# Kernel optimization log

Hardware: AMD Instinct MI355X
Metric: run time of the kernel (lower is better)

Reference implementation:

```python
import jax, jax.numpy as jnp
import numpy as np

B, T, N = 16, 2048, 24
K, C_IN, C0, C1 = 3, 1, 64, 64
KS, PRED_LEN = 3, 24
EPS = 1e-5


def _norm_laplacian(adj):
    # L = D^-1/2 A^T D^-1/2 (matches scipy path: (A D^-1/2)^T D^-1/2)
    d = adj.sum(axis=1)
    dis = jnp.where(d > 0, 1.0 / jnp.sqrt(d), 0.0)
    return dis[:, None] * adj.T * dis[None, :]


def _cheb_stack(L, k_terms):
    polys = [jnp.eye(N, dtype=L.dtype), L]
    for _ in range(2, k_terms):
        polys.append(2.0 * L @ polys[-1] - polys[-2])
    return jnp.stack(polys[:k_terms])  # (K, N, N)


def _causal_conv(x, w, b, dilation):
    ks = w.shape[-1]
    pad = (ks - 1) * dilation
    x = jnp.pad(x, ((0, 0), (0, 0), (0, 0), (pad, 0)))
    y = jax.lax.conv_general_dilated(
        x, w, window_strides=(1, 1), padding='VALID',
        rhs_dilation=(1, dilation),
        dimension_numbers=('NCHW', 'OIHW', 'NCHW'))
    return y + b[None, :, None, None]


def _bn(x, g, be):
    # training-mode batch norm over (B, N, T) per channel
    mu = x.mean(axis=(0, 2, 3), keepdims=True)
    var = x.var(axis=(0, 2, 3), keepdims=True)
    return g[None, :, None, None] * (x - mu) * jax.lax.rsqrt(var + EPS) + be[None, :, None, None]


def setup_inputs() -> dict:
    key = jax.random.key(0)
    ks = jax.random.split(key, 16)
    s = 0.05
    return {
        'batch_x': jax.random.normal(ks[0], (B, T, N), jnp.float32),
        'adj': jax.random.uniform(ks[1], (N, N), jnp.float32),
        'theta': jax.random.normal(ks[2], (K, C_IN, C0), jnp.float32),  # Theta per Cheb term
        'w1a': jax.random.normal(ks[3], (C0, C0, 1, KS), jnp.float32) * s,
        'b1a': jnp.zeros((C0,), jnp.float32),
        'g1a': jnp.ones((C0,), jnp.float32), 'be1a': jnp.zeros((C0,), jnp.float32),
        'w1b': jax.random.normal(ks[4], (C0, C0, 1, KS), jnp.float32) * s,
        'b1b': jnp.zeros((C0,), jnp.float32),
        'g1b': jnp.ones((C0,), jnp.float32), 'be1b': jnp.zeros((C0,), jnp.float32),
        'w2a': jax.random.normal(ks[5], (C1, C0, 1, KS), jnp.float32) * s,
        'b2a': jnp.zeros((C1,), jnp.float32),
        'g2a': jnp.ones((C1,), jnp.float32), 'be2a': jnp.zeros((C1,), jnp.float32),
        'w2b': jax.random.normal(ks[6], (C1, C1, 1, KS), jnp.float32) * s,
        'b2b': jnp.zeros((C1,), jnp.float32),
        'g2b': jnp.ones((C1,), jnp.float32), 'be2b': jnp.zeros((C1,), jnp.float32),
        'w_end': jax.random.normal(ks[7], (C1 // 2, C1, 1, 1), jnp.float32) * s,
        'b_end': jnp.zeros((C1 // 2,), jnp.float32),
        'w_end1': jax.random.normal(ks[8], (1, C1 // 2, 1, 2), jnp.float32) * s,
        'b_end1': jnp.zeros((1,), jnp.float32),
    }


def reference(batch_x, adj, theta,
              w1a, b1a, g1a, be1a, w1b, b1b, g1b, be1b,
              w2a, b2a, g2a, be2a, w2b, b2b, g2b, be2b,
              w_end, b_end, w_end1, b_end1):
    # (B, T, N) -> (B, 1, N, T)
    x = jnp.transpose(batch_x, (0, 2, 1))[:, None, :, :]

    # --- Cheb_conv: fused over K terms and all timesteps ---
    L = _norm_laplacian(adj)
    Tk = _cheb_stack(L, K)                       # (K, N, N)
    xp = jnp.transpose(x, (0, 2, 1, 3))          # (B, N, C_in, T)
    # out[b,o,n,t] = sum_{k,m,c} xp[b,m,c,t] Tk[k,m,n] theta[k,c,o]
    gc = jnp.einsum('bmct,kmn,kco->bont', xp, Tk, theta)  # (B, C0, N, T)

    # --- TCN block 1 (dilation 1), residual is identity (C0 == C0) ---
    h = jax.nn.relu(_bn(_causal_conv(gc, w1a, b1a, 1), g1a, be1a))
    h = jax.nn.relu(_bn(_causal_conv(h, w1b, b1b, 1), g1b, be1b))
    out0 = jax.nn.relu(h + gc)

    # --- TCN block 2 (dilation 2), residual identity (C0 == C1), no final relu ---
    h = jax.nn.relu(_bn(_causal_conv(out0, w2a, b2a, 2), g2a, be2a))
    h = jax.nn.relu(_bn(_causal_conv(h, w2b, b2b, 2), g2b, be2b))
    out = h + out0                               # (B, C1, N, T)

    # --- head: 1x1 conv + relu, then (1,2) valid conv -> 1 channel ---
    e = jax.lax.conv_general_dilated(out, w_end, (1, 1), 'VALID',
                                     dimension_numbers=('NCHW', 'OIHW', 'NCHW'))
    e = jax.nn.relu(e + b_end[None, :, None, None])
    e = jax.lax.conv_general_dilated(e, w_end1, (1, 1), 'VALID',
                                     dimension_numbers=('NCHW', 'OIHW', 'NCHW'))
    e = e + b_end1[None, :, None, None]          # (B, 1, N, T-1)
    e = e[:, 0, :, -PRED_LEN:]                   # (B, N, pred_len)
    return jnp.transpose(e, (0, 2, 1))           # (B, pred_len, N)
```

## Files before the change

kernel.cpp:

```cpp
#include <hip/hip_runtime.h>
#include <cmath>

#define TPB 256

typedef __attribute__((ext_vector_type(8)))  short short8;
typedef __attribute__((ext_vector_type(16))) float float16;

static constexpr int  BB   = 16;
static constexpr int  TDIM = 2048;
static constexpr int  NN   = 24;
static constexpr int  P    = BB * NN;
static constexpr int  C    = 64;
static constexpr int  TILE = 256;
static constexpr int  NBT  = TDIM / TILE;
static constexpr int  NSHARD = 64;
static constexpr float INV_CNT = 1.0f / 786432.0f;
static constexpr int  XPITCH = 72;

static constexpr size_t OFF_TK    = 0;
static constexpr size_t OFF_WEFF  = 6912;
static constexpr size_t OFF_WFRAG = 9216;
static constexpr size_t OFF_ST    = 82944;
static constexpr size_t OFF_BNAB  = 214016;
static constexpr size_t OFF_O0    = 216320;
static constexpr size_t OFF_YT    = 2673920;
static constexpr size_t OFF_S     = 5131520;
static constexpr size_t OFF_YA    = 14568704;
static constexpr size_t OFF_YB    = 115232000;

__device__ __forceinline__ unsigned short f2bf(float f) {
    unsigned int i = __float_as_uint(f);
    i += 0x7FFFu + ((i >> 16) & 1u);
    return (unsigned short)(i >> 16);
}
__device__ __forceinline__ float bf2f(unsigned short u) {
    return __uint_as_float((unsigned)u << 16);
}

__global__ __launch_bounds__(TPB)
void prep_kernel(const float* __restrict__ adj, const float* __restrict__ theta,
                 const float* __restrict__ w1a,
                 const float* __restrict__ w1b, const float* __restrict__ w2a,
                 const float* __restrict__ w2b,
                 float* __restrict__ tk, float* __restrict__ weff,
                 unsigned short* __restrict__ wf, float* __restrict__ stats)
{
    const int tid = threadIdx.x;
    if (blockIdx.x < 144) {
        int e = blockIdx.x * TPB + tid;
        int conv = e / 12288, r = e % 12288;
        int oh = r / 6144; r %= 6144;
        int kc = r / 512;  r %= 512;
        int lane = r / 8;
        int jj = r % 8;
        int o = oh * 32 + (lane & 31);
        int K = kc * 16 + (lane >> 5) * 8 + jj;
        int j = K / 64, c2 = K % 64;
        const float* w = (conv == 0) ? w1b : ((conv == 1) ? w2a : w2b);
        wf[e] = f2bf(w[(o * 64 + c2) * 3 + j]);
        return;
    }

    __shared__ float disl[24];
    __shared__ float Ll[576];
    __shared__ float T2l[576];

    for (int e = tid; e < 4 * 2 * 64 * NSHARD; e += TPB) stats[e] = 0.f;

    if (tid < 24) {
        float d = 0.f;
        for (int j = 0; j < 24; ++j) d += adj[tid * 24 + j];
        disl[tid] = (d > 0.f) ? 1.0f / sqrtf(d) : 0.f;
    }
    __syncthreads();
    for (int e = tid; e < 576; e += TPB) {
        int i = e / 24, j = e % 24;
        Ll[e] = disl[i] * adj[j * 24 + i] * disl[j];
    }
    __syncthreads();
    for (int e = tid; e < 576; e += TPB) {
        int i = e / 24, j = e % 24;
        float a = 0.f;
        for (int m = 0; m < 24; ++m) a += Ll[i * 24 + m] * Ll[m * 24 + j];
        T2l[e] = 2.f * a - ((i == j) ? 1.f : 0.f);
    }
    __syncthreads();
    for (int e = tid; e < 576; e += TPB) {
        int i = e / 24, j = e % 24;
        tk[e]        = (i == j) ? 1.f : 0.f;
        tk[576 + e]  = Ll[e];
        tk[1152 + e] = T2l[e];
    }
    for (int e = tid; e < 576; e += TPB) {
        int o = e / 9, k = (e % 9) / 3, j = e % 3;
        float a = 0.f;
        for (int c2 = 0; c2 < 64; ++c2)
            a += w1a[(o * 64 + c2) * 3 + j] * theta[k * 64 + c2];
        weff[(k * 3 + j) * 64 + o] = a;
    }
}

__global__ __launch_bounds__(TPB)
void bnprep_kernel(const float* __restrict__ stats, const float* __restrict__ g,
                   const float* __restrict__ be, float2* __restrict__ ab)
{
    const int tid = threadIdx.x;
    const int ch = tid >> 2, q = tid & 3;
    float s1 = 0.f, s2 = 0.f;
    #pragma unroll
    for (int u = 0; u < 16; ++u) {
        int sh = q * 16 + u;
        s1 += stats[ch * 64 + sh];
        s2 += stats[(64 + ch) * 64 + sh];
    }
    s1 += __shfl_xor(s1, 1); s1 += __shfl_xor(s1, 2);
    s2 += __shfl_xor(s2, 1); s2 += __shfl_xor(s2, 2);
    if (q == 0) {
        float mu  = s1 * INV_CNT;
        float var = s2 * INV_CNT - mu * mu;
        float a = g[ch] * (1.0f / sqrtf(var + 1e-5f));
        ab[ch] = make_float2(a, be[ch] - mu * a);
    }
}

__global__ __launch_bounds__(TPB)
void s_kernel(const float* __restrict__ bx, const float* __restrict__ tk,
              float* __restrict__ sbuf)
{
    __shared__ float bxs[256 * 25];
    __shared__ float tkl[1728];
    const int tid = threadIdx.x;
    const int b  = blockIdx.x >> 3;
    const int t0 = (blockIdx.x & 7) * 256;

    for (int e = tid; e < 1728; e += TPB) tkl[e] = tk[e];
    for (int e = tid; e < 256 * 24; e += TPB) {
        int t = e / 24, m = e % 24;
        bxs[t * 25 + m] = bx[((long)b * TDIM + t0 + t) * NN + m];
    }
    __syncthreads();

    const int t = tid;
    for (int k = 0; k < 3; ++k) {
        float acc[24];
        #pragma unroll
        for (int n = 0; n < 24; ++n) acc[n] = 0.f;
        for (int m = 0; m < 24; ++m) {
            float xb = bxs[t * 25 + m];
            const float* tr = tkl + k * 576 + m * 24;
            #pragma unroll
            for (int n = 0; n < 24; ++n) acc[n] = fmaf(xb, tr[n], acc[n]);
        }
        for (int n = 0; n < 24; ++n)
            sbuf[((long)k * P + b * NN + n) * TDIM + t0 + t] = acc[n];
    }
}

__global__ __launch_bounds__(TPB)
void stats1a_kernel(const float* __restrict__ sbuf, const float* __restrict__ weff,
                    float* __restrict__ statsOut)
{
    __shared__ float4 ssl4[3 * 66];
    __shared__ float4 wl4[144];
    __shared__ float  part[4][2][64];
    const int tid = threadIdx.x;
    const int blk = blockIdx.x;
    const int p  = blk >> 3;
    const int t0 = (blk & 7) * TILE;

    for (int e = tid; e < 576; e += TPB) ((float*)wl4)[e] = weff[e];
    for (int e = tid; e < 3 * 65; e += TPB) {
        int k = e / 65, u4 = e % 65;
        int t = t0 - 4 + u4 * 4;
        float4 v = make_float4(0.f, 0.f, 0.f, 0.f);
        if (t >= 0) v = *(const float4*)(sbuf + ((long)k * P + p) * TDIM + t);
        ssl4[k * 66 + u4] = v;
    }
    __syncthreads();

    const int oq = tid & 7;
    const int tq = tid >> 3;
    float acc[8][8];
    #pragma unroll
    for (int i = 0; i < 8; ++i)
        #pragma unroll
        for (int ti = 0; ti < 8; ++ti) acc[i][ti] = 0.f;

    #pragma unroll
    for (int k = 0; k < 3; ++k) {
        float4 x0 = ssl4[k * 66 + tq * 2];
        float4 x1 = ssl4[k * 66 + tq * 2 + 1];
        float4 x2 = ssl4[k * 66 + tq * 2 + 2];
        float xv[12] = { x0.x,x0.y,x0.z,x0.w, x1.x,x1.y,x1.z,x1.w, x2.x,x2.y,x2.z,x2.w };
        #pragma unroll
        for (int j = 0; j < 3; ++j) {
            float4 w0 = wl4[(k * 3 + j) * 16 + oq * 2];
            float4 w1 = wl4[(k * 3 + j) * 16 + oq * 2 + 1];
            float wv[8] = { w0.x,w0.y,w0.z,w0.w, w1.x,w1.y,w1.z,w1.w };
            #pragma unroll
            for (int i = 0; i < 8; ++i)
                #pragma unroll
                for (int ti = 0; ti < 8; ++ti)
                    acc[i][ti] = fmaf(wv[i], xv[ti + 2 + j], acc[i][ti]);
        }
    }

    float s1v[8], s2v[8];
    #pragma unroll
    for (int i = 0; i < 8; ++i) {
        float a1 = 0.f, a2 = 0.f;
        #pragma unroll
        for (int ti = 0; ti < 8; ++ti) { a1 += acc[i][ti]; a2 += acc[i][ti] * acc[i][ti]; }
        s1v[i] = a1; s2v[i] = a2;
    }
    #pragma unroll
    for (int m = 8; m < 64; m <<= 1) {
        #pragma unroll
        for (int i = 0; i < 8; ++i) {
            s1v[i] += __shfl_xor(s1v[i], m);
            s2v[i] += __shfl_xor(s2v[i], m);
        }
    }
    const int wave = tid >> 6, lane = tid & 63;
    if (lane < 8) {
        #pragma unroll
        for (int i = 0; i < 8; ++i) {
            part[wave][0][oq * 8 + i] = s1v[i];
            part[wave][1][oq * 8 + i] = s2v[i];
        }
    }
    __syncthreads();
    if (tid < 128) {
        int s = tid >> 6, o = tid & 63;
        float tot = part[0][s][o] + part[1][s][o] + part[2][s][o] + part[3][s][o];
        atomicAdd(&statsOut[(s * 64 + o) * NSHARD + (blk & 63)], tot);
    }
}

template<int MODE>
__global__ __launch_bounds__(TPB)
void conv_mfma(const float* __restrict__ sbuf, const unsigned short* __restrict__ yin,
               unsigned short* __restrict__ yout, float* __restrict__ ytail,
               const unsigned short* __restrict__ wf, const float* __restrict__ weff,
               const float2* __restrict__ bnab, float* __restrict__ statsOut,
               const float* __restrict__ theta, float* __restrict__ o0s)
{
    __shared__ unsigned short Xl[260 * XPITCH];
    __shared__ float4 ssl4[3 * 66];
    __shared__ float  weffl[576];
    __shared__ float  thl[192];
    __shared__ float2 abl[64];
    __shared__ float  parts[4][8][8][2];

    const int tid  = threadIdx.x;
    const int lane = tid & 63;
    const int w    = tid >> 6;
    const int oh   = w & 1;
    const int l31  = lane & 31;
    const int h    = lane >> 5;
    const int blk  = blockIdx.x;
    const int p    = blk >> 3;
    const int tile = blk & 7;
    const int t0   = tile * TILE;
    const float* sslf = (const float*)ssl4;

    short8 af[12];
    #pragma unroll
    for (int kc = 0; kc < 12; ++kc)
        af[kc] = *((const short8*)wf + (oh * 12 + kc) * 64 + lane);

    if (tid < 64) abl[tid] = bnab[tid];
    if (MODE == 0)
        for (int e = tid; e < 576; e += TPB) weffl[e] = weff[e];
    if (MODE == 1)
        for (int e = tid; e < 192; e += TPB) thl[e] = theta[e];
    if (MODE <= 1) {
        for (int e = tid; e < 3 * 66; e += TPB) {
            int k = e / 66, u4 = e % 66;
            int t = t0 - 8 + u4 * 4;
            float4 v = make_float4(0.f, 0.f, 0.f, 0.f);
            if (t >= 0) v = *(const float4*)(sbuf + ((long)k * P + p) * TDIM + t);
            ssl4[k * 66 + u4] = v;
        }
    }
    __syncthreads();

    for (int e = tid; e < 260 * 8; e += TPB) {
        const int tt = e >> 3, cb = e & 7;
        const int t = t0 - 4 + tt;
        float xv[8];
        if (t < 0) {
            #pragma unroll
            for (int r = 0; r < 8; ++r) xv[r] = 0.f;
        } else if (MODE == 0) {
            float sv[9];
            #pragma unroll
            for (int k = 0; k < 3; ++k)
                #pragma unroll
                for (int j = 0; j < 3; ++j)
                    sv[k * 3 + j] = sslf[k * 264 + tt + 2 + j];
            #pragma unroll
            for (int r = 0; r < 8; ++r) {
                int c = cb * 8 + r;
                float raw = 0.f;
                #pragma unroll
                for (int q = 0; q < 9; ++q)
                    raw = fmaf(weffl[q * 64 + c], sv[q], raw);
                float2 ab = abl[c];
                xv[r] = fmaxf(fmaf(ab.x, raw, ab.y), 0.f);
            }
        } else {
            short8 yv8 = *(const short8*)(yin + ((long)p * TDIM + t) * 64 + cb * 8);
            float gcb[3];
            if (MODE == 1) {
                gcb[0] = sslf[      tt + 4];
                gcb[1] = sslf[264 + tt + 4];
                gcb[2] = sslf[528 + tt + 4];
            }
            #pragma unroll
            for (int r = 0; r < 8; ++r) {
                int c = cb * 8 + r;
                float2 ab = abl[c];
                float v = bf2f((unsigned short)yv8[r]);
                float hh = fmaxf(fmaf(ab.x, v, ab.y), 0.f);
                if (MODE == 1) {
                    float gc = thl[c] * gcb[0] + thl[64 + c] * gcb[1] + thl[128 + c] * gcb[2];
                    hh = fmaxf(hh + gc, 0.f);
                }
                xv[r] = hh;
            }
        }
        if (MODE == 1 && tile == 7 && tt >= 235) {
            #pragma unroll
            for (int r = 0; r < 8; ++r)
                o0s[(long)p * 1600 + (cb * 8 + r) * 25 + (tt - 235)] = xv[r];
        }
        short8 pk;
        #pragma unroll
        for (int r = 0; r < 8; ++r) pk[r] = (short)f2bf(xv[r]);
        *(short8*)(Xl + tt * XPITCH + cb * 8) = pk;
    }
    __syncthreads();

    float16 acc[4];
    #pragma unroll
    for (int i = 0; i < 4; ++i)
        #pragma unroll
        for (int r = 0; r < 16; ++r) acc[i][r] = 0.f;

    const int tqb = (w >> 1) * 4;
    #pragma unroll
    for (int kc = 0; kc < 12; ++kc) {
        const int j = kc >> 2;
        const int roff = (MODE == 0) ? (2 + j) : (2 * j);
        const int cbase = (kc & 3) * 16 + h * 8;
        #pragma unroll
        for (int i = 0; i < 4; ++i) {
            int row = (tqb + i) * 32 + l31 + roff;
            short8 bfr = *(const short8*)(Xl + row * XPITCH + cbase);
            acc[i] = __builtin_amdgcn_mfma_f32_32x32x16_bf16(af[kc], bfr, acc[i], 0, 0, 0);
        }
    }

    __syncthreads();

    if (MODE == 2 && tile == 7) {
        #pragma unroll
        for (int i = 0; i < 4; ++i) {
            int tg = t0 + (tqb + i) * 32 + l31;
            if (tg >= TDIM - 25) {
                #pragma unroll
                for (int r = 0; r < 16; ++r) {
                    int o = oh * 32 + (r & 3) + 8 * (r >> 2) + 4 * h;
                    ytail[((long)p * C + o) * 25 + (tg - (TDIM - 25))] = acc[i][r];
                }
            }
        }
    }

    #pragma unroll
    for (int i = 0; i < 4; ++i) {
        int tl = (tqb + i) * 32 + l31;
        #pragma unroll
        for (int q = 0; q < 4; ++q) {
            int ob = oh * 32 + 8 * q + 4 * h;
            ushort4 pk;
            pk.x = f2bf(acc[i][4 * q + 0]);
            pk.y = f2bf(acc[i][4 * q + 1]);
            pk.z = f2bf(acc[i][4 * q + 2]);
            pk.w = f2bf(acc[i][4 * q + 3]);
            *(ushort4*)(Xl + tl * XPITCH + ob) = pk;
        }
    }
    __syncthreads();

    const int cb = tid & 7;
    float s1[8], s2[8];
    #pragma unroll
    for (int r = 0; r < 8; ++r) { s1[r] = 0.f; s2[r] = 0.f; }
    for (int e = tid; e < 2048; e += TPB) {
        int tt = e >> 3;
        short8 v = *(const short8*)(Xl + tt * XPITCH + cb * 8);
        if (MODE <= 1)
            *(short8*)(yout + ((long)p * TDIM + t0 + tt) * 64 + cb * 8) = v;
        #pragma unroll
        for (int r = 0; r < 8; ++r) {
            float f = bf2f((unsigned short)v[r]);
            s1[r] += f;
            s2[r] = fmaf(f, f, s2[r]);
        }
    }
    #pragma unroll
    for (int m = 8; m <= 32; m <<= 1) {
        #pragma unroll
        for (int r = 0; r < 8; ++r) {
            s1[r] += __shfl_xor(s1[r], m);
            s2[r] += __shfl_xor(s2[r], m);
        }
    }
    if (lane < 8) {
        #pragma unroll
        for (int r = 0; r < 8; ++r) {
            parts[w][lane][r][0] = s1[r];
            parts[w][lane][r][1] = s2[r];
        }
    }
    __syncthreads();
    if (tid < 64) {
        int o = tid, cbo = o >> 3, r = o & 7;
        float t1 = parts[0][cbo][r][0] + parts[1][cbo][r][0]
                 + parts[2][cbo][r][0] + parts[3][cbo][r][0];
        float t2 = parts[0][cbo][r][1] + parts[1][cbo][r][1]
                 + parts[2][cbo][r][1] + parts[3][cbo][r][1];
        atomicAdd(&statsOut[o * NSHARD + (blk & 63)], t1);
        atomicAdd(&statsOut[(64 + o) * NSHARD + (blk & 63)], t2);
    }
}

__global__ __launch_bounds__(TPB)
void end_kernel(const float* __restrict__ ytail, const float* __restrict__ o0s,
                const float2* __restrict__ bnab, const float* __restrict__ w_end,
                const float* __restrict__ b_end, const float* __restrict__ w_end1,
                const float* __restrict__ b_end1, float* __restrict__ out)
{
    __shared__ float2 abl[64];
    __shared__ float outl[64 * 25];
    __shared__ float e1l[32 * 25];
    __shared__ float wendl[2048];
    const int tid = threadIdx.x;
    const int p = blockIdx.x;
    const int b = p / 24, n = p % 24;

    if (tid < 64) abl[tid] = bnab[tid];
    for (int e = tid; e < 2048; e += TPB) wendl[e] = w_end[e];
    __syncthreads();

    for (int e = tid; e < 1600; e += TPB) {
        int c = e / 25, tau = e % 25;
        float v = ytail[((long)p * C + c) * 25 + tau];
        float2 ab = abl[c];
        outl[e] = fmaxf(ab.x * v + ab.y, 0.f) + o0s[(long)p * 1600 + e];
    }
    __syncthreads();
    for (int e = tid; e < 800; e += TPB) {
        int q = e / 25, tau = e % 25;
        float a = b_end[q];
        for (int c = 0; c < 64; ++c)
            a = fmaf(wendl[q * 64 + c], outl[c * 25 + tau], a);
        e1l[e] = fmaxf(a, 0.f);
    }
    __syncthreads();
    if (tid < 24) {
        float a = b_end1[0];
        #pragma unroll
        for (int q = 0; q < 32; ++q)
            a += w_end1[q * 2] * e1l[q * 25 + tid] + w_end1[q * 2 + 1] * e1l[q * 25 + tid + 1];
        out[((long)b * 24 + tid) * 24 + n] = a;
    }
}

extern "C" void kernel_launch(void* const* d_in, const int* in_sizes, int n_in,
                              void* d_out, int out_size, void* d_ws, size_t ws_size,
                              hipStream_t stream)
{
    (void)in_sizes; (void)n_in; (void)out_size; (void)ws_size;
    const float* bx    = (const float*)d_in[0];
    const float* adj   = (const float*)d_in[1];
    const float* theta = (const float*)d_in[2];
    const float* w1a   = (const float*)d_in[3];
    const float* g1a   = (const float*)d_in[5];
    const float* be1a  = (const float*)d_in[6];
    const float* w1b   = (const float*)d_in[7];
    const float* g1b   = (const float*)d_in[9];
    const float* be1b  = (const float*)d_in[10];
    const float* w2a   = (const float*)d_in[11];
    const float* g2a   = (const float*)d_in[13];
    const float* be2a  = (const float*)d_in[14];
    const float* w2b   = (const float*)d_in[15];
    const float* g2b   = (const float*)d_in[17];
    const float* be2b  = (const float*)d_in[18];
    const float* wend  = (const float*)d_in[19];
    const float* bend  = (const float*)d_in[20];
    const float* wend1 = (const float*)d_in[21];
    const float* bend1 = (const float*)d_in[22];

    char* ws = (char*)d_ws;
    float*          tk    = (float*)(ws + OFF_TK);
    float*          weff  = (float*)(ws + OFF_WEFF);
    unsigned short* wf    = (unsigned short*)(ws + OFF_WFRAG);
    float*          stats = (float*)(ws + OFF_ST);
    float2*         bnab  = (float2*)(ws + OFF_BNAB);
    float*          o0s   = (float*)(ws + OFF_O0);
    float*          ytail = (float*)(ws + OFF_YT);
    float*          sb    = (float*)(ws + OFF_S);
    unsigned short* yA    = (unsigned short*)(ws + OFF_YA);
    unsigned short* yB    = (unsigned short*)(ws + OFF_YB);

    prep_kernel   <<<145, TPB, 0, stream>>>(adj, theta, w1a, w1b, w2a, w2b,
                                            tk, weff, wf, stats);
    s_kernel      <<<128, TPB, 0, stream>>>(bx, tk, sb);
    stats1a_kernel<<<P * NBT, TPB, 0, stream>>>(sb, weff, stats);
    bnprep_kernel <<<1, TPB, 0, stream>>>(stats,         g1a, be1a, bnab);

    conv_mfma<0><<<P * NBT, TPB, 0, stream>>>(
        sb, nullptr, yA, nullptr, wf, weff,
        bnab, stats + 8192, nullptr, nullptr);
    bnprep_kernel <<<1, TPB, 0, stream>>>(stats + 8192,  g1b, be1b, bnab + 64);

    conv_mfma<1><<<P * NBT, TPB, 0, stream>>>(
        sb, yA, yB, nullptr, wf + 12288, nullptr,
        bnab + 64, stats + 16384, theta, o0s);
    bnprep_kernel <<<1, TPB, 0, stream>>>(stats + 16384, g2a, be2a, bnab + 128);

    conv_mfma<2><<<P * NBT, TPB, 0, stream>>>(
        sb, yB, nullptr, ytail, wf + 24576, nullptr,
        bnab + 128, stats + 24576, nullptr, nullptr);
    bnprep_kernel <<<1, TPB, 0, stream>>>(stats + 24576, g2b, be2b, bnab + 192);

    end_kernel<<<P, TPB, 0, stream>>>(ytail, o0s, bnab + 192,
                                      wend, bend, wend1, bend1, (float*)d_out);
}
```

Measured before the change: 359.5 us.

## Fold BN stat finalisation into consumers, split s_kernel, streamline conv epilogues

Removes the four single-block bnprep launches; each conv_mfma and end_kernel block now reduces the sharded BN statistics itself into shared memory. s_kernel is split across the three Chebyshev terms for more blocks. bf16 packing uses a perm-based round-to-nearest that drops the ties-to-even correction. The final conv mode computes BN statistics directly from MFMA accumulators in registers instead of staging through LDS. This trades redundant per-block stat reductions for fewer launches and serialization points.

```diff
diff --git a/kernel.cpp b/kernel.cpp
--- a/kernel.cpp
+++ b/kernel.cpp
@@ -21,7 +21,6 @@
 static constexpr size_t OFF_WEFF  = 6912;
 static constexpr size_t OFF_WFRAG = 9216;
 static constexpr size_t OFF_ST    = 82944;
-static constexpr size_t OFF_BNAB  = 214016;
 static constexpr size_t OFF_O0    = 216320;
 static constexpr size_t OFF_YT    = 2673920;
 static constexpr size_t OFF_S     = 5131520;
@@ -35,6 +34,34 @@
 }
 __device__ __forceinline__ float bf2f(unsigned short u) {
     return __uint_as_float((unsigned)u << 16);
+}
+__device__ __forceinline__ unsigned pk2bf(float a, float b) {
+    unsigned ua = __float_as_uint(a) + 0x8000u;
+    unsigned ub = __float_as_uint(b) + 0x8000u;
+    return __builtin_amdgcn_perm(ub, ua, 0x07060302u);
+}
+
+__device__ __forceinline__
+void bn_from_stats(const float* __restrict__ statsIn, const float* __restrict__ g,
+                   const float* __restrict__ be, float2* abl, int tid)
+{
+    const int ch = tid >> 2, q = tid & 3;
+    float s1 = 0.f, s2 = 0.f;
+    #pragma unroll
+    for (int u = 0; u < 4; ++u) {
+        float4 a = *(const float4*)(statsIn + tid * 16 + u * 4);
+        float4 b = *(const float4*)(statsIn + 4096 + tid * 16 + u * 4);
+        s1 += a.x + a.y + a.z + a.w;
+        s2 += b.x + b.y + b.z + b.w;
+    }
+    s1 += __shfl_xor(s1, 1); s1 += __shfl_xor(s1, 2);
+    s2 += __shfl_xor(s2, 1); s2 += __shfl_xor(s2, 2);
+    if (q == 0) {
+        float mu  = s1 * INV_CNT;
+        float var = s2 * INV_CNT - mu * mu;
+        float a = g[ch] * (1.0f / sqrtf(var + 1e-5f));
+        abl[ch] = make_float2(a, be[ch] - mu * a);
+    }
 }
 
 __global__ __launch_bounds__(TPB)
@@ -65,7 +92,7 @@
     __shared__ float Ll[576];
     __shared__ float T2l[576];
 
-    for (int e = tid; e < 4 * 2 * 64 * NSHARD; e += TPB) stats[e] = 0.f;
+    for (int e = tid; e < 4 * 8192; e += TPB) stats[e] = 0.f;
 
     if (tid < 24) {
         float d = 0.f;
@@ -101,39 +128,19 @@
 }
 
 __global__ __launch_bounds__(TPB)
-void bnprep_kernel(const float* __restrict__ stats, const float* __restrict__ g,
-                   const float* __restrict__ be, float2* __restrict__ ab)
-{
-    const int tid = threadIdx.x;
-    const int ch = tid >> 2, q = tid & 3;
-    float s1 = 0.f, s2 = 0.f;
-    #pragma unroll
-    for (int u = 0; u < 16; ++u) {
-        int sh = q * 16 + u;
-        s1 += stats[ch * 64 + sh];
-        s2 += stats[(64 + ch) * 64 + sh];
-    }
-    s1 += __shfl_xor(s1, 1); s1 += __shfl_xor(s1, 2);
-    s2 += __shfl_xor(s2, 1); s2 += __shfl_xor(s2, 2);
-    if (q == 0) {
-        float mu  = s1 * INV_CNT;
-        float var = s2 * INV_CNT - mu * mu;
-        float a = g[ch] * (1.0f / sqrtf(var + 1e-5f));
-        ab[ch] = make_float2(a, be[ch] - mu * a);
-    }
-}
-
-__global__ __launch_bounds__(TPB)
 void s_kernel(const float* __restrict__ bx, const float* __restrict__ tk,
               float* __restrict__ sbuf)
 {
     __shared__ float bxs[256 * 25];
-    __shared__ float tkl[1728];
+    __shared__ float tkl[576];
     const int tid = threadIdx.x;
-    const int b  = blockIdx.x >> 3;
-    const int t0 = (blockIdx.x & 7) * 256;
-
-    for (int e = tid; e < 1728; e += TPB) tkl[e] = tk[e];
+    const int blk = blockIdx.x;
+    const int b  = blk / 24;
+    const int r  = blk % 24;
+    const int k  = r >> 3;
+    const int t0 = (r & 7) * 256;
+
+    for (int e = tid; e < 576; e += TPB) tkl[e] = tk[k * 576 + e];
     for (int e = tid; e < 256 * 24; e += TPB) {
         int t = e / 24, m = e % 24;
         bxs[t * 25 + m] = bx[((long)b * TDIM + t0 + t) * NN + m];
@@ -141,19 +148,17 @@
     __syncthreads();
 
     const int t = tid;
-    for (int k = 0; k < 3; ++k) {
-        float acc[24];
-        #pragma unroll
-        for (int n = 0; n < 24; ++n) acc[n] = 0.f;
-        for (int m = 0; m < 24; ++m) {
-            float xb = bxs[t * 25 + m];
-            const float* tr = tkl + k * 576 + m * 24;
-            #pragma unroll
-            for (int n = 0; n < 24; ++n) acc[n] = fmaf(xb, tr[n], acc[n]);
-        }
-        for (int n = 0; n < 24; ++n)
-            sbuf[((long)k * P + b * NN + n) * TDIM + t0 + t] = acc[n];
-    }
+    float acc[24];
+    #pragma unroll
+    for (int n = 0; n < 24; ++n) acc[n] = 0.f;
+    for (int m = 0; m < 24; ++m) {
+        float xb = bxs[t * 25 + m];
+        const float* tr = tkl + m * 24;
+        #pragma unroll
+        for (int n = 0; n < 24; ++n) acc[n] = fmaf(xb, tr[n], acc[n]);
+    }
+    for (int n = 0; n < 24; ++n)
+        sbuf[((long)k * P + b * NN + n) * TDIM + t0 + t] = acc[n];
 }
 
 __global__ __launch_bounds__(TPB)
@@ -166,7 +171,7 @@
     const int tid = threadIdx.x;
     const int blk = blockIdx.x;
     const int p  = blk >> 3;
-    const int t0 = (blk & 7) * TILE;
+    const int t0 = (blk & 7) * 256;
 
     for (int e = tid; e < 576; e += TPB) ((float*)wl4)[e] = weff[e];
     for (int e = tid; e < 3 * 65; e += TPB) {
@@ -242,15 +247,16 @@
 void conv_mfma(const float* __restrict__ sbuf, const unsigned short* __restrict__ yin,
                unsigned short* __restrict__ yout, float* __restrict__ ytail,
                const unsigned short* __restrict__ wf, const float* __restrict__ weff,
-               const float2* __restrict__ bnab, float* __restrict__ statsOut,
+               const float* __restrict__ statsIn, const float* __restrict__ g,
+               const float* __restrict__ be, float* __restrict__ statsOut,
                const float* __restrict__ theta, float* __restrict__ o0s)
 {
     __shared__ unsigned short Xl[260 * XPITCH];
-    __shared__ float4 ssl4[3 * 66];
-    __shared__ float  weffl[576];
-    __shared__ float  thl[192];
+    __shared__ float  ssl[(MODE <= 1) ? 3 * 264 : 4];
+    __shared__ float  weffl[(MODE == 0) ? 576 : 4];
+    __shared__ float  thl[(MODE == 1) ? 192 : 4];
     __shared__ float2 abl[64];
-    __shared__ float  parts[4][8][8][2];
+    __shared__ float  parts[(MODE <= 1) ? 4 * 8 * 8 * 2 : 4 * 2 * 16 * 2];
 
     const int tid  = threadIdx.x;
     const int lane = tid & 63;
@@ -262,14 +268,14 @@
     const int p    = blk >> 3;
     const int tile = blk & 7;
     const int t0   = tile * TILE;
-    const float* sslf = (const float*)ssl4;
 
     short8 af[12];
     #pragma unroll
     for (int kc = 0; kc < 12; ++kc)
         af[kc] = *((const short8*)wf + (oh * 12 + kc) * 64 + lane);
 
-    if (tid < 64) abl[tid] = bnab[tid];
+    bn_from_stats(statsIn, g, be, abl, tid);
+
     if (MODE == 0)
         for (int e = tid; e < 576; e += TPB) weffl[e] = weff[e];
     if (MODE == 1)
@@ -280,11 +286,13 @@
             int t = t0 - 8 + u4 * 4;
             float4 v = make_float4(0.f, 0.f, 0.f, 0.f);
             if (t >= 0) v = *(const float4*)(sbuf + ((long)k * P + p) * TDIM + t);
-            ssl4[k * 66 + u4] = v;
-        }
-    }
-    __syncthreads();
-
+            *(float4*)(ssl + k * 264 + u4 * 4) = v;
+        }
+    }
+    __syncthreads();
+
+    const unsigned short* yinb = (MODE >= 1)
+        ? (yin + ((long)p * TDIM + t0 - 4) * 64) : nullptr;
     for (int e = tid; e < 260 * 8; e += TPB) {
         const int tt = e >> 3, cb = e & 7;
         const int t = t0 - 4 + tt;
@@ -298,7 +306,7 @@
             for (int k = 0; k < 3; ++k)
                 #pragma unroll
                 for (int j = 0; j < 3; ++j)
-                    sv[k * 3 + j] = sslf[k * 264 + tt + 2 + j];
+                    sv[k * 3 + j] = ssl[k * 264 + tt + 2 + j];
             #pragma unroll
             for (int r = 0; r < 8; ++r) {
                 int c = cb * 8 + r;
@@ -310,12 +318,12 @@
                 xv[r] = fmaxf(fmaf(ab.x, raw, ab.y), 0.f);
             }
         } else {
-            short8 yv8 = *(const short8*)(yin + ((long)p * TDIM + t) * 64 + cb * 8);
+            short8 yv8 = *(const short8*)(yinb + (long)e * 8);
             float gcb[3];
             if (MODE == 1) {
-                gcb[0] = sslf[      tt + 4];
-                gcb[1] = sslf[264 + tt + 4];
-                gcb[2] = sslf[528 + tt + 4];
+                gcb[0] = ssl[      tt + 4];
+                gcb[1] = ssl[264 + tt + 4];
+                gcb[2] = ssl[528 + tt + 4];
             }
             #pragma unroll
             for (int r = 0; r < 8; ++r) {
@@ -335,10 +343,12 @@
             for (int r = 0; r < 8; ++r)
                 o0s[(long)p * 1600 + (cb * 8 + r) * 25 + (tt - 235)] = xv[r];
         }
-        short8 pk;
-        #pragma unroll
-        for (int r = 0; r < 8; ++r) pk[r] = (short)f2bf(xv[r]);
-        *(short8*)(Xl + tt * XPITCH + cb * 8) = pk;
+        uint4 pk;
+        pk.x = pk2bf(xv[0], xv[1]);
+        pk.y = pk2bf(xv[2], xv[3]);
+        pk.z = pk2bf(xv[4], xv[5]);
+        pk.w = pk2bf(xv[6], xv[7]);
+        *(uint4*)(Xl + tt * XPITCH + cb * 8) = pk;
     }
     __syncthreads();
 
@@ -362,84 +372,124 @@
         }
     }
 
-    __syncthreads();
-
-    if (MODE == 2 && tile == 7) {
+    if (MODE <= 1) {
+        __syncthreads();
+
         #pragma unroll
         for (int i = 0; i < 4; ++i) {
-            int tg = t0 + (tqb + i) * 32 + l31;
-            if (tg >= TDIM - 25) {
-                #pragma unroll
-                for (int r = 0; r < 16; ++r) {
-                    int o = oh * 32 + (r & 3) + 8 * (r >> 2) + 4 * h;
-                    ytail[((long)p * C + o) * 25 + (tg - (TDIM - 25))] = acc[i][r];
+            int tl = (tqb + i) * 32 + l31;
+            #pragma unroll
+            for (int q = 0; q < 4; ++q) {
+                int ob = oh * 32 + 8 * q + 4 * h;
+                uint2 pk;
+                pk.x = pk2bf(acc[i][4 * q + 0], acc[i][4 * q + 1]);
+                pk.y = pk2bf(acc[i][4 * q + 2], acc[i][4 * q + 3]);
+                *(uint2*)(Xl + tl * XPITCH + ob) = pk;
+            }
+        }
+        __syncthreads();
+
+        const int cb = tid & 7;
+        unsigned short* youtb = yout + ((long)p * TDIM + t0) * 64;
+        float s1[8], s2[8];
+        #pragma unroll
+        for (int r = 0; r < 8; ++r) { s1[r] = 0.f; s2[r] = 0.f; }
+        for (int e = tid; e < 2048; e += TPB) {
+            int tt = e >> 3;
+            uint4 v = *(const uint4*)(Xl + tt * XPITCH + cb * 8);
+            *(uint4*)(youtb + (long)e * 8) = v;
+            unsigned uu[4] = { v.x, v.y, v.z, v.w };
+            #pragma unroll
+            for (int q = 0; q < 4; ++q) {
+                float f0 = __uint_as_float(uu[q] << 16);
+                float f1 = __uint_as_float(uu[q] & 0xFFFF0000u);
+                s1[2 * q]     += f0;  s2[2 * q]     = fmaf(f0, f0, s2[2 * q]);
+                s1[2 * q + 1] += f1;  s2[2 * q + 1] = fmaf(f1, f1, s2[2 * q + 1]);
+            }
+        }
+        #pragma unroll
+        for (int m = 8; m <= 32; m <<= 1) {
+            #pragma unroll
+            for (int r = 0; r < 8; ++r) {
+                s1[r] += __shfl_xor(s1[r], m);
+                s2[r] += __shfl_xor(s2[r], m);
+            }
+        }
+        if (lane < 8) {
+            #pragma unroll
+            for (int r = 0; r < 8; ++r) {
+                parts[((w * 8 + lane) * 8 + r) * 2 + 0] = s1[r];
+                parts[((w * 8 + lane) * 8 + r) * 2 + 1] = s2[r];
+            }
+        }
+        __syncthreads();
+        if (tid < 64) {
+            int o = tid, cbo = o >> 3, r = o & 7;
+            float t1 = 0.f, t2 = 0.f;
+            #pragma unroll
+            for (int ww = 0; ww < 4; ++ww) {
+                t1 += parts[((ww * 8 + cbo) * 8 + r) * 2 + 0];
+                t2 += parts[((ww * 8 + cbo) * 8 + r) * 2 + 1];
+            }
+            atomicAdd(&statsOut[o * NSHARD + (blk & 63)], t1);
+            atomicAdd(&statsOut[(64 + o) * NSHARD + (blk & 63)], t2);
+        }
+    } else {
+        if (tile == 7) {
+            #pragma unroll
+            for (int i = 0; i < 4; ++i) {
+                int tg = t0 + (tqb + i) * 32 + l31;
+                if (tg >= TDIM - 25) {
+                    #pragma unroll
+                    for (int r = 0; r < 16; ++r) {
+                        int o = oh * 32 + (r & 3) + 8 * (r >> 2) + 4 * h;
+                        ytail[((long)p * C + o) * 25 + (tg - (TDIM - 25))] = acc[i][r];
+                    }
                 }
             }
         }
-    }
-
-    #pragma unroll
-    for (int i = 0; i < 4; ++i) {
-        int tl = (tqb + i) * 32 + l31;
-        #pragma unroll
-        for (int q = 0; q < 4; ++q) {
-            int ob = oh * 32 + 8 * q + 4 * h;
-            ushort4 pk;
-            pk.x = f2bf(acc[i][4 * q + 0]);
-            pk.y = f2bf(acc[i][4 * q + 1]);
-            pk.z = f2bf(acc[i][4 * q + 2]);
-            pk.w = f2bf(acc[i][4 * q + 3]);
-            *(ushort4*)(Xl + tl * XPITCH + ob) = pk;
-        }
-    }
-    __syncthreads();
-
-    const int cb = tid & 7;
-    float s1[8], s2[8];
-    #pragma unroll
-    for (int r = 0; r < 8; ++r) { s1[r] = 0.f; s2[r] = 0.f; }
-    for (int e = tid; e < 2048; e += TPB) {
-        int tt = e >> 3;
-        short8 v = *(const short8*)(Xl + tt * XPITCH + cb * 8);
-        if (MODE <= 1)
-            *(short8*)(yout + ((long)p * TDIM + t0 + tt) * 64 + cb * 8) = v;
-        #pragma unroll
-        for (int r = 0; r < 8; ++r) {
-            float f = bf2f((unsigned short)v[r]);
-            s1[r] += f;
-            s2[r] = fmaf(f, f, s2[r]);
-        }
-    }
-    #pragma unroll
-    for (int m = 8; m <= 32; m <<= 1) {
-        #pragma unroll
-        for (int r = 0; r < 8; ++r) {
-            s1[r] += __shfl_xor(s1[r], m);
-            s2[r] += __shfl_xor(s2[r], m);
-        }
-    }
-    if (lane < 8) {
-        #pragma unroll
-        for (int r = 0; r < 8; ++r) {
-            parts[w][lane][r][0] = s1[r];
-            parts[w][lane][r][1] = s2[r];
-        }
-    }
-    __syncthreads();
-    if (tid < 64) {
-        int o = tid, cbo = o >> 3, r = o & 7;
-        float t1 = parts[0][cbo][r][0] + parts[1][cbo][r][0]
-                 + parts[2][cbo][r][0] + parts[3][cbo][r][0];
-        float t2 = parts[0][cbo][r][1] + parts[1][cbo][r][1]
-                 + parts[2][cbo][r][1] + parts[3][cbo][r][1];
-        atomicAdd(&statsOut[o * NSHARD + (blk & 63)], t1);
-        atomicAdd(&statsOut[(64 + o) * NSHARD + (blk & 63)], t2);
+        float s1[16], s2[16];
+        #pragma unroll
+        for (int r = 0; r < 16; ++r) {
+            float a1 = 0.f, a2 = 0.f;
+            #pragma unroll
+            for (int i = 0; i < 4; ++i) { float v = acc[i][r]; a1 += v; a2 = fmaf(v, v, a2); }
+            s1[r] = a1; s2[r] = a2;
+        }
+        #pragma unroll
+        for (int m = 1; m <= 16; m <<= 1) {
+            #pragma unroll
+            for (int r = 0; r < 16; ++r) {
+                s1[r] += __shfl_xor(s1[r], m);
+                s2[r] += __shfl_xor(s2[r], m);
+            }
+        }
+        if (l31 == 0) {
+            #pragma unroll
+            for (int r = 0; r < 16; ++r) {
+                parts[(((w * 2 + h) * 16) + r) * 2 + 0] = s1[r];
+                parts[(((w * 2 + h) * 16) + r) * 2 + 1] = s2[r];
+            }
+        }
+        __syncthreads();
+        if (tid < 64) {
+            int o = tid;
+            int ohh = o >> 5, v = o & 31;
+            int hh = (v >> 2) & 1, r = (v & 3) + 4 * (v >> 3);
+            float t1 = parts[(((ohh * 2 + hh) * 16) + r) * 2 + 0]
+                     + parts[((((ohh + 2) * 2 + hh) * 16) + r) * 2 + 0];
+            float t2 = parts[(((ohh * 2 + hh) * 16) + r) * 2 + 1]
+                     + parts[((((ohh + 2) * 2 + hh) * 16) + r) * 2 + 1];
+            atomicAdd(&statsOut[o * NSHARD + (blk & 63)], t1);
+            atomicAdd(&statsOut[(64 + o) * NSHARD + (blk & 63)], t2);
+        }
     }
 }
 
 __global__ __launch_bounds__(TPB)
 void end_kernel(const float* __restrict__ ytail, const float* __restrict__ o0s,
-                const float2* __restrict__ bnab, const float* __restrict__ w_end,
+                const float* __restrict__ statsIn, const float* __restrict__ g,
+                const float* __restrict__ be, const float* __restrict__ w_end,
                 const float* __restrict__ b_end, const float* __restrict__ w_end1,
                 const float* __restrict__ b_end1, float* __restrict__ out)
 {
@@ -451,7 +501,7 @@
     const int p = blockIdx.x;
     const int b = p / 24, n = p % 24;
 
-    if (tid < 64) abl[tid] = bnab[tid];
+    bn_from_stats(statsIn, g, be, abl, tid);
     for (int e = tid; e < 2048; e += TPB) wendl[e] = w_end[e];
     __syncthreads();
 
@@ -509,7 +559,6 @@
     float*          weff  = (float*)(ws + OFF_WEFF);
     unsigned short* wf    = (unsigned short*)(ws + OFF_WFRAG);
     float*          stats = (float*)(ws + OFF_ST);
-    float2*         bnab  = (float2*)(ws + OFF_BNAB);
     float*          o0s   = (float*)(ws + OFF_O0);
     float*          ytail = (float*)(ws + OFF_YT);
     float*          sb    = (float*)(ws + OFF_S);
@@ -518,25 +567,19 @@
 
     prep_kernel   <<<145, TPB, 0, stream>>>(adj, theta, w1a, w1b, w2a, w2b,
                                             tk, weff, wf, stats);
-    s_kernel      <<<128, TPB, 0, stream>>>(bx, tk, sb);
+    s_kernel      <<<384, TPB, 0, stream>>>(bx, tk, sb);
     stats1a_kernel<<<P * NBT, TPB, 0, stream>>>(sb, weff, stats);
-    bnprep_kernel <<<1, TPB, 0, stream>>>(stats,         g1a, be1a, bnab);
 
     conv_mfma<0><<<P * NBT, TPB, 0, stream>>>(
         sb, nullptr, yA, nullptr, wf, weff,
-        bnab, stats + 8192, nullptr, nullptr);
-    bnprep_kernel <<<1, TPB, 0, stream>>>(stats + 8192,  g1b, be1b, bnab + 64);
-
+        stats, g1a, be1a, stats + 8192, nullptr, nullptr);
     conv_mfma<1><<<P * NBT, TPB, 0, stream>>>(
         sb, yA, yB, nullptr, wf + 12288, nullptr,
-        bnab + 64, stats + 16384, theta, o0s);
-    bnprep_kernel <<<1, TPB, 0, stream>>>(stats + 16384, g2a, be2a, bnab + 128);
-
+        stats + 8192, g1b, be1b, stats + 16384, theta, o0s);
     conv_mfma<2><<<P * NBT, TPB, 0, stream>>>(
         sb, yB, nullptr, ytail, wf + 24576, nullptr,
-        bnab + 128, stats + 24576, nullptr, nullptr);
-    bnprep_kernel <<<1, TPB, 0, stream>>>(stats + 24576, g2b, be2b, bnab + 192);
-
-    end_kernel<<<P, TPB, 0, stream>>>(ytail, o0s, bnab + 192,
+        stats + 16384, g2a, be2a, stats + 24576, nullptr, nullptr);
+
+    end_kernel<<<P, TPB, 0, stream>>>(ytail, o0s, stats + 24576, g2b, be2b,
                                       wend, bend, wend1, bend1, (float*)d_out);
 }
```

Result: no change. 363.1 us (+1.0%).
